# Kernel tuning notes

Measured on AMD Instinct MI355X. Metric: run time of the kernel, lower is better.

The kernel has to match this reference:

```python
import jax, jax.numpy as jnp
import numpy as np
import math

B, T, D, K, V = 8, 2048, 512, 512, 512


def setup_inputs() -> dict:
    key = jax.random.key(0)
    ks = jax.random.split(key, 4)
    minibatch = jax.random.normal(ks[0], (B, T, D), dtype=jnp.float32)
    # nn.Linear weights are [out, in]; biases [out]
    Wk = jax.random.normal(ks[1], (K, D), dtype=jnp.float32) * 0.02
    bk = jnp.zeros((K,), dtype=jnp.float32)
    Wq = jax.random.normal(ks[2], (K, D), dtype=jnp.float32) * 0.02
    bq = jnp.zeros((K,), dtype=jnp.float32)
    Wv = jax.random.normal(ks[3], (V, D), dtype=jnp.float32) * 0.02
    bv = jnp.zeros((V,), dtype=jnp.float32)
    return {"minibatch": minibatch, "Wk": Wk, "bk": bk, "Wq": Wq, "bq": bq, "Wv": Wv, "bv": bv}


def reference(minibatch, Wk, bk, Wq, bq, Wv, bv):
    k_size = Wk.shape[0]
    sqrt_k = math.sqrt(k_size)
    keys = jnp.einsum('btd,kd->btk', minibatch, Wk) + bk
    queries = jnp.einsum('btd,kd->btk', minibatch, Wq) + bq
    values = jnp.einsum('btd,vd->btv', minibatch, Wv) + bv
    # logits[b, t, s] = q_t . k_s
    logits = jnp.einsum('btk,bsk->bts', queries, keys)
    seq = minibatch.shape[1]
    # upper triangle (s > t) masked to -inf, matching np.triu(..., k=1)
    mask = jnp.triu(jnp.ones((seq, seq), dtype=bool), k=1)
    logits = jnp.where(mask[None, :, :], -jnp.inf, logits)
    # NOTE: original softmaxes over dim=1 (the query axis), then divides by sqrt(k)
    probs = jax.nn.softmax(logits, axis=1) / sqrt_k
    read = jnp.einsum('bts,bsv->btv', probs, values)
    return minibatch + read
```

## Files before the change

kernel.cpp:

```cpp
#include <hip/hip_runtime.h>


typedef __attribute__((ext_vector_type(4))) float f32x4;
typedef __attribute__((ext_vector_type(8))) short s16x8;
typedef __attribute__((ext_vector_type(4))) short s16x4;

#define SQRTK  22.627416997969522f

__device__ __forceinline__ float bf2f(unsigned short u) {
    union { unsigned int i; float f; } c; c.i = ((unsigned int)u) << 16; return c.f;
}
__device__ __forceinline__ short f2bf(float f) {
    union { float f; unsigned int i; } c; c.f = f;
    unsigned int x = c.i;
    return (short)((x + 0x7fffu + ((x >> 16) & 1u)) >> 16);
}
__device__ __forceinline__ void gll16(const void* g, void* l) {
    __builtin_amdgcn_global_load_lds(
        (const __attribute__((address_space(1))) void*)g,
        (__attribute__((address_space(3))) void*)l, 16, 0, 0);
}

__global__ __launch_bounds__(256) void k_cast(
    const float* __restrict__ in, unsigned short* __restrict__ out, int n4)
{
    int i = blockIdx.x * 256 + threadIdx.x;
    if (i >= n4) return;
    f32x4 v = *(const f32x4*)(in + (size_t)i * 4);
    s16x4 o;
#pragma unroll
    for (int j = 0; j < 4; ++j) o[j] = f2bf(v[j]);
    *(s16x4*)(out + (size_t)i * 4) = o;
}

__global__ __launch_bounds__(256) void k_castw(
    const float* __restrict__ q, const float* __restrict__ k, const float* __restrict__ v,
    unsigned short* __restrict__ oqk, unsigned short* __restrict__ ov)
{
    int i = blockIdx.x * 256 + threadIdx.x;
    const float* src; unsigned short* dst; int j;
    if (i < 65536)       { src = q; dst = oqk; j = i; }
    else if (i < 131072) { src = k; dst = oqk + 262144; j = i - 65536; }
    else                 { src = v; dst = ov; j = i - 131072; }
    f32x4 w = *(const f32x4*)(src + (size_t)j * 4);
    s16x4 o;
#pragma unroll
    for (int jj = 0; jj < 4; ++jj) o[jj] = f2bf(w[jj]);
    *(s16x4*)(dst + (size_t)j * 4) = o;
}

__global__ __launch_bounds__(256) void k_projqk(
    const unsigned short* __restrict__ Xb,
    const unsigned short* __restrict__ Wqk,
    const float* __restrict__ bq, const float* __restrict__ bk,
    unsigned short* __restrict__ C)
{
    __shared__ short la[2][128][32];
    __shared__ short lb[2][128][32];
    const int tid  = threadIdx.x;
    const int wave = tid >> 6, lane = tid & 63;
    const int wr = (wave >> 1) * 64, wc = (wave & 1) * 64;
    const int m0 = blockIdx.x * 128, n0 = blockIdx.y * 128;
    const int r0 = tid >> 2, c0 = (tid & 3) * 8;
    const int wvb = wave * 1024;
    const int frl = lane & 15, kb = (lane >> 4) * 8, rg4 = (lane >> 4) * 4;
    f32x4 acc[4][4] = {};

#define QK_STAGE(BUF, K0) { \
    char* pa_ = (char*)(&la[BUF][0][0]) + wvb; \
    char* pb_ = (char*)(&lb[BUF][0][0]) + wvb; \
    gll16(Xb  + (size_t)(m0 + r0) * 512 + (K0) + c0, pa_); \
    gll16(Xb  + (size_t)(m0 + r0 + 64) * 512 + (K0) + c0, pa_ + 4096); \
    gll16(Wqk + (size_t)(n0 + r0) * 512 + (K0) + c0, pb_); \
    gll16(Wqk + (size_t)(n0 + r0 + 64) * 512 + (K0) + c0, pb_ + 4096); }

    QK_STAGE(0, 0);
    __syncthreads();
    for (int ks = 0; ks < 16; ++ks) {
        const int cur = ks & 1;
        if (ks < 15) QK_STAGE(cur ^ 1, (ks + 1) * 32);
        s16x8 af[4], bfr[4];
#pragma unroll
        for (int i = 0; i < 4; ++i) af[i]  = *(const s16x8*)(&la[cur][wr + i * 16 + frl][kb]);
#pragma unroll
        for (int i = 0; i < 4; ++i) bfr[i] = *(const s16x8*)(&lb[cur][wc + i * 16 + frl][kb]);
#pragma unroll
        for (int mi = 0; mi < 4; ++mi)
#pragma unroll
            for (int ni = 0; ni < 4; ++ni)
                acc[mi][ni] = __builtin_amdgcn_mfma_f32_16x16x32_bf16(af[mi], bfr[ni], acc[mi][ni], 0, 0, 0);
        __syncthreads();
    }
#undef QK_STAGE
#pragma unroll
    for (int mi = 0; mi < 4; ++mi)
#pragma unroll
        for (int ni = 0; ni < 4; ++ni) {
            int col = n0 + wc + ni * 16 + frl;
            float bv = (col < 512) ? bq[col] : bk[col - 512];
#pragma unroll
            for (int r = 0; r < 4; ++r) {
                int row = m0 + wr + mi * 16 + rg4 + r;
                C[(size_t)row * 1024 + col] = f2bf(acc[mi][ni][r] + bv);
            }
        }
}

__global__ __launch_bounds__(256) void k_projv(
    const unsigned short* __restrict__ Wv,
    const unsigned short* __restrict__ Xb,
    const float* __restrict__ bv,
    unsigned short* __restrict__ C)
{
    __shared__ short la[2][128][32];
    __shared__ short lb[2][128][32];
    const int tid  = threadIdx.x;
    const int wave = tid >> 6, lane = tid & 63;
    const int wr = (wave >> 1) * 64, wc = (wave & 1) * 64;
    const int m0 = blockIdx.x * 128, n0 = blockIdx.y * 128;
    const int r0 = tid >> 2, c0 = (tid & 3) * 8;
    const int wvb = wave * 1024;
    const int frl = lane & 15, kb = (lane >> 4) * 8, rg4 = (lane >> 4) * 4;
    f32x4 acc[4][4] = {};

#define PV_STAGE(BUF, K0) { \
    char* pa_ = (char*)(&la[BUF][0][0]) + wvb; \
    char* pb_ = (char*)(&lb[BUF][0][0]) + wvb; \
    gll16(Wv + (size_t)(m0 + r0) * 512 + (K0) + c0, pa_); \
    gll16(Wv + (size_t)(m0 + r0 + 64) * 512 + (K0) + c0, pa_ + 4096); \
    gll16(Xb + (size_t)(n0 + r0) * 512 + (K0) + c0, pb_); \
    gll16(Xb + (size_t)(n0 + r0 + 64) * 512 + (K0) + c0, pb_ + 4096); }

    PV_STAGE(0, 0);
    __syncthreads();
    for (int ks = 0; ks < 16; ++ks) {
        const int cur = ks & 1;
        if (ks < 15) PV_STAGE(cur ^ 1, (ks + 1) * 32);
        s16x8 af[4], bfr[4];
#pragma unroll
        for (int i = 0; i < 4; ++i) af[i]  = *(const s16x8*)(&la[cur][wr + i * 16 + frl][kb]);
#pragma unroll
        for (int i = 0; i < 4; ++i) bfr[i] = *(const s16x8*)(&lb[cur][wc + i * 16 + frl][kb]);
#pragma unroll
        for (int mi = 0; mi < 4; ++mi)
#pragma unroll
            for (int ni = 0; ni < 4; ++ni)
                acc[mi][ni] = __builtin_amdgcn_mfma_f32_16x16x32_bf16(af[mi], bfr[ni], acc[mi][ni], 0, 0, 0);
        __syncthreads();
    }
#undef PV_STAGE
#pragma unroll
    for (int mi = 0; mi < 4; ++mi)
#pragma unroll
        for (int ni = 0; ni < 4; ++ni) {
            int col = n0 + wc + ni * 16 + frl;
#pragma unroll
            for (int r = 0; r < 4; ++r) {
                int row = m0 + wr + mi * 16 + rg4 + r;
                C[(size_t)row * 16384 + col] = f2bf(acc[mi][ni][r] + bv[row]);
            }
        }
}

__global__ __launch_bounds__(256) void k_logits(
    const unsigned short* __restrict__ QK,
    unsigned short* __restrict__ Pc,
    float* __restrict__ pz)
{
    const int n = blockIdx.x;
    const int b = n & 7;
    const int p = n >> 3;
    int tt = (int)((sqrtf(8.f * p + 1.f) - 1.f) * 0.5f);
    while ((tt + 1) * (tt + 2) / 2 <= p) ++tt;
    while (tt * (tt + 1) / 2 > p) --tt;
    const int st = p - tt * (tt + 1) / 2;
    const int t0 = tt * 128, s0 = st * 128;

    const unsigned short* A  = QK + (size_t)b * 2048 * 1024;
    const unsigned short* Bt = QK + (size_t)b * 2048 * 1024 + 512;
    unsigned short* Pb = Pc + (size_t)b * 2048 * 2048;

    __shared__ short la[2][128][32];
    __shared__ short lb[2][128][32];
    __shared__ float sz[2][128];
    const int tid  = threadIdx.x;
    const int wave = tid >> 6, lane = tid & 63;
    const int wr = (wave >> 1) * 64, wc = (wave & 1) * 64;
    const int r0 = tid >> 2, c0 = (tid & 3) * 8;
    const int wvb = wave * 1024;
    const int frl = lane & 15, kb = (lane >> 4) * 8, rg4 = (lane >> 4) * 4;
    f32x4 acc[4][4] = {};

#define LG_STAGE(BUF, K0) { \
    char* pa_ = (char*)(&la[BUF][0][0]) + wvb; \
    char* pb_ = (char*)(&lb[BUF][0][0]) + wvb; \
    gll16(A  + (size_t)(t0 + r0) * 1024 + (K0) + c0, pa_); \
    gll16(A  + (size_t)(t0 + r0 + 64) * 1024 + (K0) + c0, pa_ + 4096); \
    gll16(Bt + (size_t)(s0 + r0) * 1024 + (K0) + c0, pb_); \
    gll16(Bt + (size_t)(s0 + r0 + 64) * 1024 + (K0) + c0, pb_ + 4096); }

    LG_STAGE(0, 0);
    __syncthreads();
    for (int ks = 0; ks < 16; ++ks) {
        const int cur = ks & 1;
        if (ks < 15) LG_STAGE(cur ^ 1, (ks + 1) * 32);
        s16x8 af[4], bfr[4];
#pragma unroll
        for (int i = 0; i < 4; ++i) af[i]  = *(const s16x8*)(&la[cur][wr + i * 16 + frl][kb]);
#pragma unroll
        for (int i = 0; i < 4; ++i) bfr[i] = *(const s16x8*)(&lb[cur][wc + i * 16 + frl][kb]);
#pragma unroll
        for (int mi = 0; mi < 4; ++mi)
#pragma unroll
            for (int ni = 0; ni < 4; ++ni)
                acc[mi][ni] = __builtin_amdgcn_mfma_f32_16x16x32_bf16(af[mi], bfr[ni], acc[mi][ni], 0, 0, 0);
        __syncthreads();
    }
#undef LG_STAGE

    float cz[4];
#pragma unroll
    for (int ni = 0; ni < 4; ++ni) {
        const int colg = s0 + wc + ni * 16 + frl;
        float zl = 0.f;
#pragma unroll
        for (int mi = 0; mi < 4; ++mi)
#pragma unroll
            for (int r = 0; r < 4; ++r) {
                int row = t0 + wr + mi * 16 + rg4 + r;
                float e = (colg <= row) ? __expf(acc[mi][ni][r]) : 0.f;
                acc[mi][ni][r] = e;
                zl += e;
            }
        zl += __shfl_xor(zl, 16);
        zl += __shfl_xor(zl, 32);
        cz[ni] = zl;
    }
    if (lane < 16) {
#pragma unroll
        for (int ni = 0; ni < 4; ++ni)
            sz[wr >> 6][wc + ni * 16 + lane] = cz[ni];
    }
    __syncthreads();
    if (tid < 128)
        pz[(b * 16 + tt) * 2048 + s0 + tid] = sz[0][tid] + sz[1][tid];
#pragma unroll
    for (int ni = 0; ni < 4; ++ni) {
        const int colg = s0 + wc + ni * 16 + frl;
#pragma unroll
        for (int mi = 0; mi < 4; ++mi)
#pragma unroll
            for (int r = 0; r < 4; ++r) {
                int row = t0 + wr + mi * 16 + rg4 + r;
                Pb[(size_t)row * 2048 + colg] = f2bf(acc[mi][ni][r]);
            }
    }
}

__global__ __launch_bounds__(256) void k_stats2(
    const float* __restrict__ pz, float* __restrict__ ft)
{
    const int i = blockIdx.x * 256 + threadIdx.x;
    const int b = i >> 11, s = i & 2047;
    float Z = 0.f;
    for (int tc = s >> 7; tc < 16; ++tc) Z += pz[(b * 16 + tc) * 2048 + s];
    ft[i] = 1.0f / (Z * SQRTK);
}

__global__ __launch_bounds__(256) void k_out(
    const unsigned short* __restrict__ Pc,
    const float* __restrict__ ft,
    const unsigned short* __restrict__ Vt,
    const float* __restrict__ X,
    float* __restrict__ Y)
{
    __shared__ short la[2][2][128][32];
    __shared__ short lb[2][2][128][32];
    const int n  = blockIdx.x;
    const int tt = 15 - (n >> 5);
    const int bv = n & 31;
    const int b = bv >> 2, v = bv & 3;
    const int t0 = tt * 128, v0 = v * 128;
    const unsigned short* Pb = Pc + (size_t)b * 2048 * 2048;
    const float* fb = ft + (size_t)b * 2048;
    const int tid  = threadIdx.x;
    const int wave = tid >> 6, lane = tid & 63;
    const int wr = (wave >> 1) * 64, wc = (wave & 1) * 64;
    const int frl = lane & 15, kb = (lane >> 4) * 8, rg4 = (lane >> 4) * 4;

    const int rA  = tid >> 2;
    const int cA  = (tid & 3) * 8;

    f32x4 acc[4][4] = {};
    s16x8 pa[4], vb[4];
    f32x4 f4[4];
    const int nit = (tt + 1) * 2;

#define OUT_LOAD(IT) { \
    int sb = (IT) * 64; \
    const unsigned short* pp = Pb + (size_t)(t0 + rA) * 2048 + sb + cA; \
    pa[0] = *(const s16x8*)(pp); \
    pa[1] = *(const s16x8*)(pp + (size_t)64 * 2048); \
    pa[2] = *(const s16x8*)(pp + 32); \
    pa[3] = *(const s16x8*)(pp + (size_t)64 * 2048 + 32); \
    const unsigned short* vp = Vt + (size_t)(v0 + rA) * 16384 + b * 2048 + sb + cA; \
    vb[0] = *(const s16x8*)(vp); \
    vb[1] = *(const s16x8*)(vp + (size_t)64 * 16384); \
    vb[2] = *(const s16x8*)(vp + 32); \
    vb[3] = *(const s16x8*)(vp + (size_t)64 * 16384 + 32); \
    f4[0] = *(const f32x4*)(fb + sb + cA); \
    f4[1] = *(const f32x4*)(fb + sb + cA + 4); \
    f4[2] = *(const f32x4*)(fb + sb + cA + 32); \
    f4[3] = *(const f32x4*)(fb + sb + cA + 36); }

#define OUT_WRITE(BUF) { \
    s16x8 o0, o1, o2, o3; \
    _Pragma("unroll") for (int j = 0; j < 4; ++j) { \
        o0[j]     = f2bf(bf2f((unsigned short)pa[0][j])     * f4[0][j]); \
        o0[j + 4] = f2bf(bf2f((unsigned short)pa[0][j + 4]) * f4[1][j]); \
        o1[j]     = f2bf(bf2f((unsigned short)pa[1][j])     * f4[0][j]); \
        o1[j + 4] = f2bf(bf2f((unsigned short)pa[1][j + 4]) * f4[1][j]); \
        o2[j]     = f2bf(bf2f((unsigned short)pa[2][j])     * f4[2][j]); \
        o2[j + 4] = f2bf(bf2f((unsigned short)pa[2][j + 4]) * f4[3][j]); \
        o3[j]     = f2bf(bf2f((unsigned short)pa[3][j])     * f4[2][j]); \
        o3[j + 4] = f2bf(bf2f((unsigned short)pa[3][j + 4]) * f4[3][j]); } \
    *(s16x8*)(&la[BUF][0][rA][cA]) = o0; \
    *(s16x8*)(&la[BUF][0][rA + 64][cA]) = o1; \
    *(s16x8*)(&la[BUF][1][rA][cA]) = o2; \
    *(s16x8*)(&la[BUF][1][rA + 64][cA]) = o3; \
    *(s16x8*)(&lb[BUF][0][rA][cA]) = vb[0]; \
    *(s16x8*)(&lb[BUF][0][rA + 64][cA]) = vb[1]; \
    *(s16x8*)(&lb[BUF][1][rA][cA]) = vb[2]; \
    *(s16x8*)(&lb[BUF][1][rA + 64][cA]) = vb[3]; }

    OUT_LOAD(0);
    OUT_WRITE(0);
    __syncthreads();
    for (int it = 0; it < nit; ++it) {
        const int cur = it & 1;
        if (it + 1 < nit) OUT_LOAD(it + 1);
#pragma unroll
        for (int h = 0; h < 2; ++h) {
            s16x8 af[4], bfr[4];
#pragma unroll
            for (int i = 0; i < 4; ++i) af[i]  = *(const s16x8*)(&la[cur][h][wr + i * 16 + frl][kb]);
#pragma unroll
            for (int i = 0; i < 4; ++i) bfr[i] = *(const s16x8*)(&lb[cur][h][wc + i * 16 + frl][kb]);
#pragma unroll
            for (int mi = 0; mi < 4; ++mi)
#pragma unroll
                for (int ni = 0; ni < 4; ++ni)
                    acc[mi][ni] = __builtin_amdgcn_mfma_f32_16x16x32_bf16(af[mi], bfr[ni], acc[mi][ni], 0, 0, 0);
        }
        if (it + 1 < nit) OUT_WRITE(cur ^ 1);
        __syncthreads();
    }
#undef OUT_LOAD
#undef OUT_WRITE

#pragma unroll
    for (int mi = 0; mi < 4; ++mi)
#pragma unroll
        for (int ni = 0; ni < 4; ++ni) {
            int col = v0 + wc + ni * 16 + frl;
#pragma unroll
            for (int r = 0; r < 4; ++r) {
                int row = t0 + wr + mi * 16 + rg4 + r;
                size_t o = ((size_t)b * 2048 + row) * 512 + col;
                Y[o] = acc[mi][ni][r] + X[o];
            }
        }
}

extern "C" void kernel_launch(void* const* d_in, const int* in_sizes, int n_in,
                              void* d_out, int out_size, void* d_ws, size_t ws_size,
                              hipStream_t stream) {
    const float* Xf  = (const float*)d_in[0];
    const float* Wkf = (const float*)d_in[1];
    const float* bkf = (const float*)d_in[2];
    const float* Wqf = (const float*)d_in[3];
    const float* bqf = (const float*)d_in[4];
    const float* Wvf = (const float*)d_in[5];
    const float* bvf = (const float*)d_in[6];
    float* Y = (float*)d_out;
    char* ws = (char*)d_ws;

    float*          pz   = (float*)(ws);
    float*          ftab = (float*)(ws + 2097152);
    unsigned short* Wqkb = (unsigned short*)(ws + 4194304);
    unsigned short* Wvb  = (unsigned short*)(ws + 5242880);
    unsigned short* Xb   = (unsigned short*)(ws + 6291456);
    unsigned short* QKb  = (unsigned short*)(ws + 23068672);
    unsigned short* Vt   = (unsigned short*)(ws + 56623104);
    unsigned short* Pc   = (unsigned short*)(ws + 73400320);

    dim3 blk(256);
    k_cast<<<dim3(8192), blk, 0, stream>>>(Xf, Xb, 2097152);
    k_castw<<<dim3(768), blk, 0, stream>>>(Wqf, Wkf, Wvf, Wqkb, Wvb);
    k_projqk<<<dim3(128, 8), blk, 0, stream>>>(Xb, Wqkb, bqf, bkf, QKb);
    k_projv<<<dim3(4, 128), blk, 0, stream>>>(Wvb, Xb, bvf, Vt);
    k_logits<<<dim3(1088), blk, 0, stream>>>(QKb, Pc, pz);
    k_stats2<<<dim3(64), blk, 0, stream>>>(pz, ftab);
    k_out<<<dim3(512), blk, 0, stream>>>(Pc, ftab, Vt, Xf, Y);
}
```

Before: 146.0 us.

## Fold softmax column scale into V projection and stage k_out via direct LDS loads

Moves the per-key normalization factor (1/(Z*sqrtK)) out of the k_out inner loop and into the V projection epilogue, so V is pre-scaled per key position. k_projv is reordered to run after k_stats2 so the factors are ready. With no per-element rescaling of P left, k_out now stages P and V tiles straight into LDS with global_load_lds instead of going through registers and converting bf16 to float and back. This removes VALU work and register pressure from the main attention GEMM. The cost is an extra rounding of V after scaling and a serialized dependency of the V projection on the stats kernel.

```diff
diff --git a/kernel.cpp b/kernel.cpp
--- a/kernel.cpp
+++ b/kernel.cpp
@@ -7,9 +7,6 @@
 
 #define SQRTK  22.627416997969522f
 
-__device__ __forceinline__ float bf2f(unsigned short u) {
-    union { unsigned int i; float f; } c; c.i = ((unsigned int)u) << 16; return c.f;
-}
 __device__ __forceinline__ short f2bf(float f) {
     union { float f; unsigned int i; } c; c.f = f;
     unsigned int x = c.i;
@@ -110,6 +107,7 @@
     const unsigned short* __restrict__ Wv,
     const unsigned short* __restrict__ Xb,
     const float* __restrict__ bv,
+    const float* __restrict__ ft,
     unsigned short* __restrict__ C)
 {
     __shared__ short la[2][128][32];
@@ -154,10 +152,11 @@
 #pragma unroll
         for (int ni = 0; ni < 4; ++ni) {
             int col = n0 + wc + ni * 16 + frl;
+            float fs = ft[col];
 #pragma unroll
             for (int r = 0; r < 4; ++r) {
                 int row = m0 + wr + mi * 16 + rg4 + r;
-                C[(size_t)row * 16384 + col] = f2bf(acc[mi][ni][r] + bv[row]);
+                C[(size_t)row * 16384 + col] = f2bf((acc[mi][ni][r] + bv[row]) * fs);
             }
         }
 }
@@ -269,8 +268,7 @@
 
 __global__ __launch_bounds__(256) void k_out(
     const unsigned short* __restrict__ Pc,
-    const float* __restrict__ ft,
-    const unsigned short* __restrict__ Vt,
+    const unsigned short* __restrict__ Vs,
     const float* __restrict__ X,
     float* __restrict__ Y)
 {
@@ -282,63 +280,31 @@
     const int b = bv >> 2, v = bv & 3;
     const int t0 = tt * 128, v0 = v * 128;
     const unsigned short* Pb = Pc + (size_t)b * 2048 * 2048;
-    const float* fb = ft + (size_t)b * 2048;
     const int tid  = threadIdx.x;
     const int wave = tid >> 6, lane = tid & 63;
     const int wr = (wave >> 1) * 64, wc = (wave & 1) * 64;
     const int frl = lane & 15, kb = (lane >> 4) * 8, rg4 = (lane >> 4) * 4;
-
-    const int rA  = tid >> 2;
-    const int cA  = (tid & 3) * 8;
+    const int r0 = tid >> 2, c0 = (tid & 3) * 8;
+    const int wvb = wave * 1024;
 
     f32x4 acc[4][4] = {};
-    s16x8 pa[4], vb[4];
-    f32x4 f4[4];
     const int nit = (tt + 1) * 2;
 
-#define OUT_LOAD(IT) { \
+#define OUT_STAGE(BUF, IT) { \
     int sb = (IT) * 64; \
-    const unsigned short* pp = Pb + (size_t)(t0 + rA) * 2048 + sb + cA; \
-    pa[0] = *(const s16x8*)(pp); \
-    pa[1] = *(const s16x8*)(pp + (size_t)64 * 2048); \
-    pa[2] = *(const s16x8*)(pp + 32); \
-    pa[3] = *(const s16x8*)(pp + (size_t)64 * 2048 + 32); \
-    const unsigned short* vp = Vt + (size_t)(v0 + rA) * 16384 + b * 2048 + sb + cA; \
-    vb[0] = *(const s16x8*)(vp); \
-    vb[1] = *(const s16x8*)(vp + (size_t)64 * 16384); \
-    vb[2] = *(const s16x8*)(vp + 32); \
-    vb[3] = *(const s16x8*)(vp + (size_t)64 * 16384 + 32); \
-    f4[0] = *(const f32x4*)(fb + sb + cA); \
-    f4[1] = *(const f32x4*)(fb + sb + cA + 4); \
-    f4[2] = *(const f32x4*)(fb + sb + cA + 32); \
-    f4[3] = *(const f32x4*)(fb + sb + cA + 36); }
-
-#define OUT_WRITE(BUF) { \
-    s16x8 o0, o1, o2, o3; \
-    _Pragma("unroll") for (int j = 0; j < 4; ++j) { \
-        o0[j]     = f2bf(bf2f((unsigned short)pa[0][j])     * f4[0][j]); \
-        o0[j + 4] = f2bf(bf2f((unsigned short)pa[0][j + 4]) * f4[1][j]); \
-        o1[j]     = f2bf(bf2f((unsigned short)pa[1][j])     * f4[0][j]); \
-        o1[j + 4] = f2bf(bf2f((unsigned short)pa[1][j + 4]) * f4[1][j]); \
-        o2[j]     = f2bf(bf2f((unsigned short)pa[2][j])     * f4[2][j]); \
-        o2[j + 4] = f2bf(bf2f((unsigned short)pa[2][j + 4]) * f4[3][j]); \
-        o3[j]     = f2bf(bf2f((unsigned short)pa[3][j])     * f4[2][j]); \
-        o3[j + 4] = f2bf(bf2f((unsigned short)pa[3][j + 4]) * f4[3][j]); } \
-    *(s16x8*)(&la[BUF][0][rA][cA]) = o0; \
-    *(s16x8*)(&la[BUF][0][rA + 64][cA]) = o1; \
-    *(s16x8*)(&la[BUF][1][rA][cA]) = o2; \
-    *(s16x8*)(&la[BUF][1][rA + 64][cA]) = o3; \
-    *(s16x8*)(&lb[BUF][0][rA][cA]) = vb[0]; \
-    *(s16x8*)(&lb[BUF][0][rA + 64][cA]) = vb[1]; \
-    *(s16x8*)(&lb[BUF][1][rA][cA]) = vb[2]; \
-    *(s16x8*)(&lb[BUF][1][rA + 64][cA]) = vb[3]; }
-
-    OUT_LOAD(0);
-    OUT_WRITE(0);
+    _Pragma("unroll") for (int h = 0; h < 2; ++h) { \
+        char* pa_ = (char*)(&la[BUF][h][0][0]) + wvb; \
+        char* pb_ = (char*)(&lb[BUF][h][0][0]) + wvb; \
+        gll16(Pb + (size_t)(t0 + r0) * 2048 + sb + h * 32 + c0, pa_); \
+        gll16(Pb + (size_t)(t0 + r0 + 64) * 2048 + sb + h * 32 + c0, pa_ + 4096); \
+        gll16(Vs + (size_t)(v0 + r0) * 16384 + b * 2048 + sb + h * 32 + c0, pb_); \
+        gll16(Vs + (size_t)(v0 + r0 + 64) * 16384 + b * 2048 + sb + h * 32 + c0, pb_ + 4096); } }
+
+    OUT_STAGE(0, 0);
     __syncthreads();
     for (int it = 0; it < nit; ++it) {
         const int cur = it & 1;
-        if (it + 1 < nit) OUT_LOAD(it + 1);
+        if (it + 1 < nit) OUT_STAGE(cur ^ 1, it + 1);
 #pragma unroll
         for (int h = 0; h < 2; ++h) {
             s16x8 af[4], bfr[4];
@@ -352,11 +318,9 @@
                 for (int ni = 0; ni < 4; ++ni)
                     acc[mi][ni] = __builtin_amdgcn_mfma_f32_16x16x32_bf16(af[mi], bfr[ni], acc[mi][ni], 0, 0, 0);
         }
-        if (it + 1 < nit) OUT_WRITE(cur ^ 1);
         __syncthreads();
     }
-#undef OUT_LOAD
-#undef OUT_WRITE
+#undef OUT_STAGE
 
 #pragma unroll
     for (int mi = 0; mi < 4; ++mi)
@@ -391,15 +355,15 @@
     unsigned short* Wvb  = (unsigned short*)(ws + 5242880);
     unsigned short* Xb   = (unsigned short*)(ws + 6291456);
     unsigned short* QKb  = (unsigned short*)(ws + 23068672);
-    unsigned short* Vt   = (unsigned short*)(ws + 56623104);
+    unsigned short* Vs   = (unsigned short*)(ws + 56623104);
     unsigned short* Pc   = (unsigned short*)(ws + 73400320);
 
     dim3 blk(256);
     k_cast<<<dim3(8192), blk, 0, stream>>>(Xf, Xb, 2097152);
     k_castw<<<dim3(768), blk, 0, stream>>>(Wqf, Wkf, Wvf, Wqkb, Wvb);
     k_projqk<<<dim3(128, 8), blk, 0, stream>>>(Xb, Wqkb, bqf, bkf, QKb);
-    k_projv<<<dim3(4, 128), blk, 0, stream>>>(Wvb, Xb, bvf, Vt);
     k_logits<<<dim3(1088), blk, 0, stream>>>(QKb, Pc, pz);
     k_stats2<<<dim3(64), blk, 0, stream>>>(pz, ftab);
-    k_out<<<dim3(512), blk, 0, stream>>>(Pc, ftab, Vt, Xf, Y);
-}
+    k_projv<<<dim3(4, 128), blk, 0, stream>>>(Wvb, Xb, bvf, ftab, Vs);
+    k_out<<<dim3(512), blk, 0, stream>>>(Pc, Vs, Xf, Y);
+}
```

Measured after the change: 144.5 us. Within noise of the previous version (-1.1%).
